# Performance work log

Measured on AMD Instinct MI355X. Metric: run time of the kernel, lower is better.

## Reference

```python
import jax, jax.numpy as jnp
import numpy as np

B, L, D = 8, 4096, 512
H, DK = 8, 64           # num_heads, key_dim = D // H
SAMPLE_K = 512
CONV_K = 3
POOL = 2


def setup_inputs() -> dict:
    key = jax.random.key(0)
    ks = jax.random.split(key, 8)
    x = jax.random.normal(ks[0], (B, L, D), dtype=jnp.float32)
    sample_indices = jax.random.randint(ks[1], (SAMPLE_K,), 0, L, dtype=jnp.int32)
    s = 1.0 / np.sqrt(D)
    Wq = jax.random.uniform(ks[2], (D, H * DK), jnp.float32, -s, s)
    Wk = jax.random.uniform(ks[3], (D, H * DK), jnp.float32, -s, s)
    Wv = jax.random.uniform(ks[4], (D, H * DK), jnp.float32, -s, s)
    conv_w = jax.random.normal(ks[5], (CONV_K, H * DK, H * DK), jnp.float32) * 0.02
    conv_b = jnp.zeros((H * DK,), jnp.float32)
    comb_w = jax.random.normal(ks[6], (H * DK, D), jnp.float32) * 0.02
    comb_b = jnp.zeros((D,), jnp.float32)
    return {"x": x, "Wq": Wq, "Wk": Wk, "Wv": Wv, "conv_w": conv_w,
            "conv_b": conv_b, "comb_w": comb_w, "comb_b": comb_b,
            "sample_indices": sample_indices}


def reference(x, Wq, Wk, Wv, conv_w, conv_b, comb_w, comb_b, sample_indices):
    b, l, _ = x.shape
    # QKV projections -> [B, H, L, DK]
    Q = (x @ Wq).reshape(b, l, H, DK).transpose(0, 2, 1, 3)
    K = (x @ Wk).reshape(b, l, H, DK).transpose(0, 2, 1, 3)
    V = (x @ Wv).reshape(b, l, H, DK).transpose(0, 2, 1, 3)
    # sample K/V along sequence axis -> [B, H, S, DK]
    Ks = jnp.take(K, sample_indices, axis=2)
    Vs = jnp.take(V, sample_indices, axis=2)
    # scores [B, H, L, S]
    scores = jnp.einsum('bhld,bhsd->bhls', Q, Ks) / jnp.sqrt(jnp.float32(DK))
    # second gather along the sampled axis (size S); indices in [0, L) so
    # out-of-range indices are clipped (JAX default), matching jit-safe semantics
    scores = jnp.take(scores, sample_indices, axis=3, mode='clip')
    attn = jax.nn.softmax(scores, axis=-1)
    out = jnp.einsum('bhls,bhsd->bhld', attn, Vs)          # [B, H, L, DK]
    out = out.transpose(0, 2, 1, 3).reshape(b, l, H * DK)  # [B, L, E]
    # Conv1D, padding SAME, NWC / WIO
    out = jax.lax.conv_general_dilated(
        out, conv_w, window_strides=(1,), padding='SAME',
        dimension_numbers=('NWC', 'WIO', 'NWC')) + conv_b
    out = jax.nn.elu(out)
    # MaxPool1D: pool == stride, L divisible by POOL
    out = out.reshape(b, l // POOL, POOL, H * DK).max(axis=2)
    # combine heads (Dense back to D); Dropout is identity at inference
    out = out @ comb_w + comb_b
    return out
```

## Files before the change

### kernel.cpp

```cpp
#include <hip/hip_runtime.h>


typedef __attribute__((ext_vector_type(8))) short  short8;
typedef __attribute__((ext_vector_type(4))) short  short4b;
typedef __attribute__((ext_vector_type(4))) float  f32x4;

#define LSEQ   4096
#define SK     512
#define EDIM   512
#define LPAD   4098
#define PADROW 2098176
#define SCALE2 0.180336880f

static __device__ __forceinline__ float bf2f(unsigned short h) {
    union { unsigned int u; float f; } v; v.u = ((unsigned int)h) << 16; return v.f;
}
static __device__ __forceinline__ unsigned short f2bf(float f) {
    union { float f; unsigned int u; } v; v.f = f;
    unsigned int r = (v.u + 0x7fffu + ((v.u >> 16) & 1u)) >> 16;
    return (unsigned short)r;
}
static __device__ __forceinline__ unsigned int cvt_pk_bf16(float lo, float hi) {
    unsigned int r;
    asm("v_cvt_pk_bf16_f32 %0, %1, %2" : "=v"(r) : "v"(lo), "v"(hi));
    return r;
}

__global__ __launch_bounds__(256)
void cvt_bf16(const float* __restrict__ src, unsigned short* __restrict__ dst)
{
    const size_t i = ((size_t)blockIdx.x * 256 + threadIdx.x) * 8;
    const float4 a = *(const float4*)(src + i);
    const float4 b = *(const float4*)(src + i + 4);
    short8 o;
    o[0] = (short)f2bf(a.x); o[1] = (short)f2bf(a.y);
    o[2] = (short)f2bf(a.z); o[3] = (short)f2bf(a.w);
    o[4] = (short)f2bf(b.x); o[5] = (short)f2bf(b.y);
    o[6] = (short)f2bf(b.z); o[7] = (short)f2bf(b.w);
    *(short8*)(dst + i) = o;
}

__global__ __launch_bounds__(256)
void tr_f32_bf16(unsigned short* __restrict__ dst, const float* __restrict__ src,
                 int R, int C)
{
    __shared__ unsigned short T[64][72];
    const int t  = threadIdx.x;
    const int r0 = blockIdx.y * 64, c0 = blockIdx.x * 64;
    const int row = t >> 2, cg = (t & 3) * 16;
    const float* s = src + (size_t)(r0 + row) * C + c0 + cg;
    const float4 f0 = *(const float4*)s;
    const float4 f1 = *(const float4*)(s + 4);
    const float4 f2 = *(const float4*)(s + 8);
    const float4 f3 = *(const float4*)(s + 12);
    T[row][cg + 0]  = f2bf(f0.x); T[row][cg + 1]  = f2bf(f0.y);
    T[row][cg + 2]  = f2bf(f0.z); T[row][cg + 3]  = f2bf(f0.w);
    T[row][cg + 4]  = f2bf(f1.x); T[row][cg + 5]  = f2bf(f1.y);
    T[row][cg + 6]  = f2bf(f1.z); T[row][cg + 7]  = f2bf(f1.w);
    T[row][cg + 8]  = f2bf(f2.x); T[row][cg + 9]  = f2bf(f2.y);
    T[row][cg + 10] = f2bf(f2.z); T[row][cg + 11] = f2bf(f2.w);
    T[row][cg + 12] = f2bf(f3.x); T[row][cg + 13] = f2bf(f3.y);
    T[row][cg + 14] = f2bf(f3.z); T[row][cg + 15] = f2bf(f3.w);
    __syncthreads();
    unsigned short* d = dst + (size_t)(c0 + row) * R + r0 + cg;
    short8 o0, o1;
    #pragma unroll
    for (int k = 0; k < 8; ++k) o0[k] = (short)T[cg + k][row];
    #pragma unroll
    for (int k = 0; k < 8; ++k) o1[k] = (short)T[cg + 8 + k][row];
    *(short8*)d       = o0;
    *(short8*)(d + 8) = o1;
}

__global__ __launch_bounds__(256)
void tr_bf16(unsigned short* __restrict__ dst, const unsigned short* __restrict__ src,
             int R, int C)
{
    __shared__ unsigned short T[64][72];
    const size_t bofs = (size_t)blockIdx.z * (size_t)R * (size_t)C;
    src += bofs; dst += bofs;
    const int t  = threadIdx.x;
    const int r0 = blockIdx.y * 64, c0 = blockIdx.x * 64;
    const int row = t >> 2, cg = (t & 3) * 16;
    const unsigned short* s = src + (size_t)(r0 + row) * C + c0 + cg;
    *(short8*)&T[row][cg]     = *(const short8*)s;
    *(short8*)&T[row][cg + 8] = *(const short8*)(s + 8);
    __syncthreads();
    unsigned short* d = dst + (size_t)(c0 + row) * R + r0 + cg;
    short8 o0, o1;
    #pragma unroll
    for (int k = 0; k < 8; ++k) o0[k] = (short)T[cg + k][row];
    #pragma unroll
    for (int k = 0; k < 8; ++k) o1[k] = (short)T[cg + 8 + k][row];
    *(short8*)d       = o0;
    *(short8*)(d + 8) = o1;
}

__global__ __launch_bounds__(256)
void gather_rows(const unsigned short* __restrict__ xb, const int* __restrict__ sidx,
                 unsigned short* __restrict__ xkg, unsigned short* __restrict__ xvg)
{
    const int blk = blockIdx.x;
    const int b = blk >> 9, j = blk & 511;
    const int t = threadIdx.x;
    int qv = sidx[j];               qv = qv < 0 ? 0 : (qv > LSEQ - 1 ? LSEQ - 1 : qv);
    int cv = qv < SK - 1 ? qv : SK - 1;
    int pv = sidx[cv];              pv = pv < 0 ? 0 : (pv > LSEQ - 1 ? LSEQ - 1 : pv);
    const unsigned int* xs = (const unsigned int*)xb;
    unsigned int* kd = (unsigned int*)xkg;
    unsigned int* vd = (unsigned int*)xvg;
    const size_t dst = ((size_t)b * SK + j) * 256 + t;
    kd[dst] = xs[((size_t)b * LSEQ + pv) * 256 + t];
    vd[dst] = xs[((size_t)b * LSEQ + qv) * 256 + t];
}

__global__ __launch_bounds__(256)
void zero_pad(unsigned short* __restrict__ attpad)
{
    const int i = blockIdx.x * 256 + threadIdx.x;
    const int b = i >> 9, c = i & 511;
    attpad[(size_t)b * PADROW + c] = 0;
    attpad[(size_t)b * PADROW + (size_t)(LPAD - 1) * 512 + c] = 0;
}

template<int MODE>
__global__ __launch_bounds__(256)
void gemm128(const unsigned short* __restrict__ A, const unsigned short* __restrict__ Bt,
             const float* __restrict__ bias, void* __restrict__ Cout, int K)
{
    __shared__ unsigned short As[128 * 40];
    __shared__ unsigned short Bs[128 * 40];
    const int t    = threadIdx.x;
    const int n0   = blockIdx.x * 128;
    const int m0   = blockIdx.y * 128;
    const int srow = t >> 1, scg = (t & 1) * 16;
    const int lane = t & 63, wv = t >> 6;
    const int q = lane >> 4, ln = lane & 15;
    const int wm = (wv & 1) * 64, wn = (wv >> 1) * 64;

    const unsigned short* abase;
    if (MODE == 1) {
        const int gr = m0 + srow;
        abase = A + (size_t)(gr >> 12) * PADROW + (size_t)(gr & 4095) * 512;
    } else {
        abase = A + (size_t)(m0 + srow) * K;
    }
    const unsigned short* bbase = Bt + (size_t)(n0 + srow) * K;

    const f32x4 zero = {0.f, 0.f, 0.f, 0.f};
    f32x4 acc[4][4];
    #pragma unroll
    for (int i = 0; i < 4; ++i)
        #pragma unroll
        for (int j = 0; j < 4; ++j) acc[i][j] = zero;

    short8 av0 = *(const short8*)(abase + scg);
    short8 av1 = *(const short8*)(abase + scg + 8);
    short8 bv0 = *(const short8*)(bbase + scg);
    short8 bv1 = *(const short8*)(bbase + scg + 8);

    for (int k0 = 0; k0 < K; k0 += 32) {
        __syncthreads();
        *(short8*)&As[srow * 40 + scg]     = av0;
        *(short8*)&As[srow * 40 + scg + 8] = av1;
        *(short8*)&Bs[srow * 40 + scg]     = bv0;
        *(short8*)&Bs[srow * 40 + scg + 8] = bv1;
        __syncthreads();
        if (k0 + 32 < K) {
            av0 = *(const short8*)(abase + k0 + 32 + scg);
            av1 = *(const short8*)(abase + k0 + 32 + scg + 8);
            bv0 = *(const short8*)(bbase + k0 + 32 + scg);
            bv1 = *(const short8*)(bbase + k0 + 32 + scg + 8);
        }
        short8 af[4], bf[4];
        #pragma unroll
        for (int mt = 0; mt < 4; ++mt)
            af[mt] = *(const short8*)&As[(wm + mt * 16 + ln) * 40 + q * 8];
        #pragma unroll
        for (int nt = 0; nt < 4; ++nt)
            bf[nt] = *(const short8*)&Bs[(wn + nt * 16 + ln) * 40 + q * 8];
        #pragma unroll
        for (int mt = 0; mt < 4; ++mt)
            #pragma unroll
            for (int nt = 0; nt < 4; ++nt)
                acc[mt][nt] = __builtin_amdgcn_mfma_f32_16x16x32_bf16(af[mt], bf[nt], acc[mt][nt], 0, 0, 0);
    }

    if (MODE == 0) {
        unsigned short* C = (unsigned short*)Cout;
        #pragma unroll
        for (int mt = 0; mt < 4; ++mt)
            #pragma unroll
            for (int r = 0; r < 4; ++r) {
                const int grow = m0 + wm + mt * 16 + q * 4 + r;
                unsigned short* cp = C + (size_t)grow * 512 + n0 + wn + ln;
                #pragma unroll
                for (int nt = 0; nt < 4; ++nt) cp[nt * 16] = f2bf(acc[mt][nt][r]);
            }
    } else if (MODE == 2) {
        float* C = (float*)Cout;
        float bb[4];
        #pragma unroll
        for (int nt = 0; nt < 4; ++nt) bb[nt] = bias[n0 + wn + nt * 16 + ln];
        #pragma unroll
        for (int mt = 0; mt < 4; ++mt)
            #pragma unroll
            for (int r = 0; r < 4; ++r) {
                const int grow = m0 + wm + mt * 16 + q * 4 + r;
                float* cp = C + (size_t)grow * 512 + n0 + wn + ln;
                #pragma unroll
                for (int nt = 0; nt < 4; ++nt) cp[nt * 16] = acc[mt][nt][r] + bb[nt];
            }
    } else {
        unsigned short* C = (unsigned short*)Cout;
        float bb[4];
        #pragma unroll
        for (int nt = 0; nt < 4; ++nt) bb[nt] = bias[n0 + wn + nt * 16 + ln];
        #pragma unroll
        for (int mt = 0; mt < 4; ++mt) {
            const int grow = m0 + wm + mt * 16 + q * 4;
            const int b = grow >> 12, l = grow & 4095;
            unsigned short* cp = C + ((size_t)b * 2048 + (l >> 1)) * 512 + n0 + wn + ln;
            #pragma unroll
            for (int nt = 0; nt < 4; ++nt) {
                float v0 = acc[mt][nt][0] + bb[nt]; v0 = v0 > 0.f ? v0 : __expf(v0) - 1.f;
                float v1 = acc[mt][nt][1] + bb[nt]; v1 = v1 > 0.f ? v1 : __expf(v1) - 1.f;
                float v2 = acc[mt][nt][2] + bb[nt]; v2 = v2 > 0.f ? v2 : __expf(v2) - 1.f;
                float v3 = acc[mt][nt][3] + bb[nt]; v3 = v3 > 0.f ? v3 : __expf(v3) - 1.f;
                cp[nt * 16]       = f2bf(fmaxf(v0, v1));
                cp[512 + nt * 16] = f2bf(fmaxf(v2, v3));
            }
        }
    }
}

__global__ __launch_bounds__(256, 2)
void attn_fused(const unsigned short* __restrict__ xb, const unsigned short* __restrict__ WqT,
                const unsigned short* __restrict__ Kg, const unsigned short* __restrict__ Vt,
                unsigned short* __restrict__ attpad)
{
    __shared__ unsigned short Ks[128][72];
    __shared__ unsigned short Vs[64][136];
    __shared__ unsigned short Pp[128][136];
    const int t = threadIdx.x;
    const int wv = t >> 6, lane = t & 63, q = lane >> 4, ln = lane & 15;
    const int l0 = blockIdx.x * 128, h = blockIdx.y, b = blockIdx.z;
    const int qr0 = wv * 32;
    const f32x4 zero = {0.f, 0.f, 0.f, 0.f};

    const unsigned short* kgb = Kg + (size_t)b * SK * 512 + h * 64;
    const unsigned short* vtb = Vt + ((size_t)(b * EDIM + h * 64)) * SK;
    const int ksr = t >> 1, ksc = (t & 1) * 32;
    const int vsr = t >> 2, vsc = (t & 3) * 32;

    short8 kp0, kp1, kp2, kp3, vp0, vp1, vp2, vp3;
    {
        const unsigned short* ks = kgb + (size_t)ksr * 512 + ksc;
        kp0 = *(const short8*)ks;        kp1 = *(const short8*)(ks + 8);
        kp2 = *(const short8*)(ks + 16); kp3 = *(const short8*)(ks + 24);
        const unsigned short* vs = vtb + (size_t)vsr * SK + vsc;
        vp0 = *(const short8*)vs;        vp1 = *(const short8*)(vs + 8);
        vp2 = *(const short8*)(vs + 16); vp3 = *(const short8*)(vs + 24);
    }

    f32x4 qacc[2][4];
    #pragma unroll
    for (int g = 0; g < 2; ++g)
        #pragma unroll
        for (int nt = 0; nt < 4; ++nt) qacc[g][nt] = zero;
    const unsigned short* xr0 = xb + ((size_t)(b * LSEQ + l0 + qr0 + ln)) * 512 + q * 8;
    const unsigned short* xr1 = xr0 + (size_t)16 * 512;
    const unsigned short* wqp = WqT + ((size_t)(h * 64 + ln)) * 512 + q * 8;
    for (int ks = 0; ks < 16; ++ks) {
        const short8 ax0 = *(const short8*)(xr0 + ks * 32);
        const short8 ax1 = *(const short8*)(xr1 + ks * 32);
        #pragma unroll
        for (int nt = 0; nt < 4; ++nt) {
            const short8 bw = *(const short8*)(wqp + nt * 16 * 512 + ks * 32);
            qacc[0][nt] = __builtin_amdgcn_mfma_f32_16x16x32_bf16(ax0, bw, qacc[0][nt], 0, 0, 0);
            qacc[1][nt] = __builtin_amdgcn_mfma_f32_16x16x32_bf16(ax1, bw, qacc[1][nt], 0, 0, 0);
        }
    }
    #pragma unroll
    for (int g = 0; g < 2; ++g)
        #pragma unroll
        for (int nt = 0; nt < 4; ++nt)
            #pragma unroll
            for (int r = 0; r < 4; ++r)
                Pp[qr0 + g * 16 + q * 4 + r][nt * 16 + ln] = f2bf(qacc[g][nt][r]);
    asm volatile("s_waitcnt lgkmcnt(0)" ::: "memory");
    short8 bq[2][2];
    #pragma unroll
    for (int g = 0; g < 2; ++g) {
        bq[g][0] = *(const short8*)&Pp[qr0 + g * 16 + ln][q * 8];
        bq[g][1] = *(const short8*)&Pp[qr0 + g * 16 + ln][q * 8 + 32];
    }

    float m_run[2] = {-1e30f, -1e30f}, l_run[2] = {0.f, 0.f};
    f32x4 o[2][4];
    #pragma unroll
    for (int g = 0; g < 2; ++g)
        #pragma unroll
        for (int j = 0; j < 4; ++j) o[g][j] = zero;

    for (int c = 0; c < 4; ++c) {
        *(short8*)&Ks[ksr][ksc]      = kp0;  *(short8*)&Ks[ksr][ksc + 8]  = kp1;
        *(short8*)&Ks[ksr][ksc + 16] = kp2;  *(short8*)&Ks[ksr][ksc + 24] = kp3;
        *(short8*)&Vs[vsr][vsc]      = vp0;  *(short8*)&Vs[vsr][vsc + 8]  = vp1;
        *(short8*)&Vs[vsr][vsc + 16] = vp2;  *(short8*)&Vs[vsr][vsc + 24] = vp3;
        __syncthreads();

        f32x4 st[8][2];
        #pragma unroll
        for (int mt = 0; mt < 8; ++mt) {
            const short8 ak0 = *(const short8*)&Ks[mt * 16 + ln][q * 8];
            const short8 ak1 = *(const short8*)&Ks[mt * 16 + ln][q * 8 + 32];
            #pragma unroll
            for (int g = 0; g < 2; ++g) {
                f32x4 a = zero;
                a = __builtin_amdgcn_mfma_f32_16x16x32_bf16(ak0, bq[g][0], a, 0, 0, 0);
                a = __builtin_amdgcn_mfma_f32_16x16x32_bf16(ak1, bq[g][1], a, 0, 0, 0);
                #pragma unroll
                for (int r = 0; r < 4; ++r) a[r] *= SCALE2;
                st[mt][g] = a;
            }
        }

        float alpha_[2];
        #pragma unroll
        for (int g = 0; g < 2; ++g) {
            float mx = st[0][g][0];
            #pragma unroll
            for (int mt = 0; mt < 8; ++mt)
                #pragma unroll
                for (int r = 0; r < 4; ++r) mx = fmaxf(mx, st[mt][g][r]);
            mx = fmaxf(mx, __shfl_xor(mx, 16));
            mx = fmaxf(mx, __shfl_xor(mx, 32));
            const float m_new = fmaxf(m_run[g], mx);
            alpha_[g] = __builtin_amdgcn_exp2f(m_run[g] - m_new);
            m_run[g] = m_new;
            float ls = 0.f;
            #pragma unroll
            for (int mt = 0; mt < 8; ++mt) {
                const float p0 = __builtin_amdgcn_exp2f(st[mt][g][0] - m_new);
                const float p1 = __builtin_amdgcn_exp2f(st[mt][g][1] - m_new);
                const float p2 = __builtin_amdgcn_exp2f(st[mt][g][2] - m_new);
                const float p3 = __builtin_amdgcn_exp2f(st[mt][g][3] - m_new);
                ls += (p0 + p1) + (p2 + p3);
                uint2 pw;
                pw.x = cvt_pk_bf16(p0, p1);
                pw.y = cvt_pk_bf16(p2, p3);
                *(uint2*)&Pp[qr0 + g * 16 + ln][mt * 16 + q * 4] = pw;
            }
            ls += __shfl_xor(ls, 16);
            ls += __shfl_xor(ls, 32);
            l_run[g] = l_run[g] * alpha_[g] + ls;
        }

        #pragma unroll
        for (int g = 0; g < 2; ++g) {
            #pragma unroll
            for (int r = 0; r < 4; ++r) {
                const float ab = __shfl(alpha_[g], q * 4 + r);
                #pragma unroll
                for (int j = 0; j < 4; ++j) o[g][j][r] *= ab;
            }
        }

        if (c < 3) {
            const unsigned short* ks = kgb + (size_t)((c + 1) * 128 + ksr) * 512 + ksc;
            kp0 = *(const short8*)ks;        kp1 = *(const short8*)(ks + 8);
            kp2 = *(const short8*)(ks + 16); kp3 = *(const short8*)(ks + 24);
            const unsigned short* vs = vtb + (size_t)vsr * SK + (c + 1) * 128 + vsc;
            vp0 = *(const short8*)vs;        vp1 = *(const short8*)(vs + 8);
            vp2 = *(const short8*)(vs + 16); vp3 = *(const short8*)(vs + 24);
        }

        asm volatile("s_waitcnt lgkmcnt(0)" ::: "memory");

        #pragma unroll
        for (int ks2 = 0; ks2 < 4; ++ks2) {
            const short8 ap0 = *(const short8*)&Pp[qr0 + ln][ks2 * 32 + q * 8];
            const short8 ap1 = *(const short8*)&Pp[qr0 + 16 + ln][ks2 * 32 + q * 8];
            #pragma unroll
            for (int j = 0; j < 4; ++j) {
                const short8 bv = *(const short8*)&Vs[j * 16 + ln][ks2 * 32 + q * 8];
                o[0][j] = __builtin_amdgcn_mfma_f32_16x16x32_bf16(ap0, bv, o[0][j], 0, 0, 0);
                o[1][j] = __builtin_amdgcn_mfma_f32_16x16x32_bf16(ap1, bv, o[1][j], 0, 0, 0);
            }
        }
        __syncthreads();
    }

    #pragma unroll
    for (int g = 0; g < 2; ++g) {
        const float li = 1.f / l_run[g];
        #pragma unroll
        for (int r = 0; r < 4; ++r) {
            const float ib = __shfl(li, q * 4 + r);
            const int rl = qr0 + g * 16 + q * 4 + r;
            #pragma unroll
            for (int j = 0; j < 4; ++j)
                attpad[((size_t)b * PADROW) + (size_t)(l0 + rl + 1) * 512 + h * 64 + j * 16 + ln]
                    = f2bf(o[g][j][r] * ib);
        }
    }
}

extern "C" void kernel_launch(void* const* d_in, const int* in_sizes, int n_in,
                              void* d_out, int out_size, void* d_ws, size_t ws_size,
                              hipStream_t stream)
{
    const float* x    = (const float*)d_in[0];
    const float* Wq   = (const float*)d_in[1];
    const float* Wk   = (const float*)d_in[2];
    const float* Wv   = (const float*)d_in[3];
    const float* cw   = (const float*)d_in[4];
    const float* cb   = (const float*)d_in[5];
    const float* mw   = (const float*)d_in[6];
    const float* mb2  = (const float*)d_in[7];
    const int*   sidx = (const int*)d_in[8];
    float* out = (float*)d_out;

    char* ws = (char*)d_ws;
    unsigned short* xb    = (unsigned short*)(ws + 0);
    unsigned short* Pool  = (unsigned short*)(ws + 0);
    unsigned short* Pad   = (unsigned short*)(ws + 33554432);
    unsigned short* xkg   = (unsigned short*)(ws + 33554432);
    unsigned short* xvg   = (unsigned short*)(ws + 37748736);
    unsigned short* Vg    = (unsigned short*)(ws + 41943040);
    unsigned short* Kg    = (unsigned short*)(ws + 67125248);
    unsigned short* Vt    = (unsigned short*)(ws + 71319552);
    unsigned short* WqT   = (unsigned short*)(ws + 75513856);
    unsigned short* WkT   = (unsigned short*)(ws + 76038144);
    unsigned short* WvT   = (unsigned short*)(ws + 76562432);
    unsigned short* CombT = (unsigned short*)(ws + 77086720);
    unsigned short* ConvT = (unsigned short*)(ws + 77611008);

    dim3 blk(256);

    cvt_bf16<<<dim3(8192), blk, 0, stream>>>(x, xb);

    tr_f32_bf16<<<dim3(8, 8),  blk, 0, stream>>>(WqT,   Wq, 512, 512);
    tr_f32_bf16<<<dim3(8, 8),  blk, 0, stream>>>(WkT,   Wk, 512, 512);
    tr_f32_bf16<<<dim3(8, 8),  blk, 0, stream>>>(WvT,   Wv, 512, 512);
    tr_f32_bf16<<<dim3(8, 8),  blk, 0, stream>>>(CombT, mw, 512, 512);
    tr_f32_bf16<<<dim3(8, 24), blk, 0, stream>>>(ConvT, cw, 1536, 512);

    gather_rows<<<dim3(4096), blk, 0, stream>>>(xb, sidx, xkg, xvg);

    gemm128<0><<<dim3(4, 32), blk, 0, stream>>>(xkg, WkT, nullptr, Kg, 512);
    gemm128<0><<<dim3(4, 32), blk, 0, stream>>>(xvg, WvT, nullptr, Vg, 512);

    tr_bf16<<<dim3(8, 8, 8), blk, 0, stream>>>(Vt, Vg, 512, 512);

    zero_pad<<<dim3(16), blk, 0, stream>>>(Pad);
    attn_fused<<<dim3(32, 8, 8), blk, 0, stream>>>(xb, WqT, Kg, Vt, Pad);

    gemm128<1><<<dim3(4, 256), blk, 0, stream>>>(Pad, ConvT, cb, Pool, 1536);

    gemm128<2><<<dim3(4, 128), blk, 0, stream>>>(Pool, CombT, mb2, out, 512);
}
```

Baseline: 384.0 us.

## Double-buffer GEMM tiles with direct global-to-LDS async loads

The tiled bf16 MFMA GEMM now loads its A and B tiles straight from global memory into LDS using the global_load_lds builtin, instead of staging them through registers. It also double-buffers the LDS tiles, so the next K-slice is fetched while the current one is consumed, and drops to one barrier per iteration. This is meant to save register traffic and a synchronisation, and to overlap memory latency with MFMA work. In exchange, the LDS row padding (stride 40) is removed to fit the 16-byte-per-lane layout, so fragment reads may hit more bank conflicts. Correctness also relies on the barrier waiting for the async LDS writes to finish.

```diff
diff --git a/kernel.cpp b/kernel.cpp
--- a/kernel.cpp
+++ b/kernel.cpp
@@ -24,6 +24,12 @@
     unsigned int r;
     asm("v_cvt_pk_bf16_f32 %0, %1, %2" : "=v"(r) : "v"(lo), "v"(hi));
     return r;
+}
+typedef __attribute__((address_space(1))) const unsigned int  gu32;
+typedef __attribute__((address_space(3))) unsigned int        lu32;
+static __device__ __forceinline__ void g2l16(const unsigned short* g, unsigned short* l)
+{
+    __builtin_amdgcn_global_load_lds((gu32*)g, (lu32*)l, 16, 0, 0);
 }
 
 __global__ __launch_bounds__(256)
@@ -128,24 +134,32 @@
 void gemm128(const unsigned short* __restrict__ A, const unsigned short* __restrict__ Bt,
              const float* __restrict__ bias, void* __restrict__ Cout, int K)
 {
-    __shared__ unsigned short As[128 * 40];
-    __shared__ unsigned short Bs[128 * 40];
+    __shared__ unsigned short As[2][128 * 32];
+    __shared__ unsigned short Bs[2][128 * 32];
     const int t    = threadIdx.x;
     const int n0   = blockIdx.x * 128;
     const int m0   = blockIdx.y * 128;
-    const int srow = t >> 1, scg = (t & 1) * 16;
     const int lane = t & 63, wv = t >> 6;
     const int q = lane >> 4, ln = lane & 15;
     const int wm = (wv & 1) * 64, wn = (wv >> 1) * 64;
 
-    const unsigned short* abase;
+    const int srl = (wv << 5) + (lane >> 2);
+    const int scs = (lane & 3) * 8;
+    const unsigned short* arow0;
+    const unsigned short* arow1;
     if (MODE == 1) {
-        const int gr = m0 + srow;
-        abase = A + (size_t)(gr >> 12) * PADROW + (size_t)(gr & 4095) * 512;
+        const int gr0 = m0 + srl;
+        arow0 = A + (size_t)(gr0 >> 12) * PADROW + (size_t)(gr0 & 4095) * 512 + scs;
+        arow1 = arow0 + (size_t)16 * 512;
     } else {
-        abase = A + (size_t)(m0 + srow) * K;
-    }
-    const unsigned short* bbase = Bt + (size_t)(n0 + srow) * K;
+        arow0 = A + (size_t)(m0 + srl) * K + scs;
+        arow1 = arow0 + (size_t)16 * K;
+    }
+    const unsigned short* brow0 = Bt + (size_t)(n0 + srl) * K + scs;
+    const unsigned short* brow1 = brow0 + (size_t)16 * K;
+
+    const int lb0 = (wv << 5) * 32;
+    const int lb1 = lb0 + 16 * 32;
 
     const f32x4 zero = {0.f, 0.f, 0.f, 0.f};
     f32x4 acc[4][4];
@@ -154,31 +168,26 @@
         #pragma unroll
         for (int j = 0; j < 4; ++j) acc[i][j] = zero;
 
-    short8 av0 = *(const short8*)(abase + scg);
-    short8 av1 = *(const short8*)(abase + scg + 8);
-    short8 bv0 = *(const short8*)(bbase + scg);
-    short8 bv1 = *(const short8*)(bbase + scg + 8);
+    g2l16(arow0, &As[0][lb0]);  g2l16(arow1, &As[0][lb1]);
+    g2l16(brow0, &Bs[0][lb0]);  g2l16(brow1, &Bs[0][lb1]);
 
     for (int k0 = 0; k0 < K; k0 += 32) {
-        __syncthreads();
-        *(short8*)&As[srow * 40 + scg]     = av0;
-        *(short8*)&As[srow * 40 + scg + 8] = av1;
-        *(short8*)&Bs[srow * 40 + scg]     = bv0;
-        *(short8*)&Bs[srow * 40 + scg + 8] = bv1;
+        const int cur = (k0 >> 5) & 1;
         __syncthreads();
         if (k0 + 32 < K) {
-            av0 = *(const short8*)(abase + k0 + 32 + scg);
-            av1 = *(const short8*)(abase + k0 + 32 + scg + 8);
-            bv0 = *(const short8*)(bbase + k0 + 32 + scg);
-            bv1 = *(const short8*)(bbase + k0 + 32 + scg + 8);
+            const int nxt = cur ^ 1;
+            g2l16(arow0 + k0 + 32, &As[nxt][lb0]);
+            g2l16(arow1 + k0 + 32, &As[nxt][lb1]);
+            g2l16(brow0 + k0 + 32, &Bs[nxt][lb0]);
+            g2l16(brow1 + k0 + 32, &Bs[nxt][lb1]);
         }
         short8 af[4], bf[4];
         #pragma unroll
         for (int mt = 0; mt < 4; ++mt)
-            af[mt] = *(const short8*)&As[(wm + mt * 16 + ln) * 40 + q * 8];
+            af[mt] = *(const short8*)&As[cur][(wm + mt * 16 + ln) * 32 + q * 8];
         #pragma unroll
         for (int nt = 0; nt < 4; ++nt)
-            bf[nt] = *(const short8*)&Bs[(wn + nt * 16 + ln) * 40 + q * 8];
+            bf[nt] = *(const short8*)&Bs[cur][(wn + nt * 16 + ln) * 32 + q * 8];
         #pragma unroll
         for (int mt = 0; mt < 4; ++mt)
             #pragma unroll
```

Result: no change. 381.6 us (-0.6%).
